# Performance work log

Hardware: AMD Instinct MI355X
Metric: run time of the kernel (lower is better)

Reference implementation:

```python
import jax, jax.numpy as jnp
import numpy as np

N_QUBITS = 8
DEPTH = 6
BATCH = 32
C = jnp.complex64

# Noise strengths from get_ibm_noise_params: constants derived from IBM Nairobi gate errors.
G1, G2 = 0.0003, 0.0065

def _amp_kraus(g):
    return [jnp.array([[1.0, 0.0], [0.0, np.sqrt(1.0 - g)]], C),
            jnp.array([[0.0, np.sqrt(g)], [0.0, 0.0]], C)]

def _phase_kraus(g):
    return [jnp.array([[1.0, 0.0], [0.0, np.sqrt(1.0 - g)]], C),
            jnp.array([[0.0, 0.0], [0.0, np.sqrt(g)]], C)]

def _depol_kraus(p):
    s0, s = np.sqrt(1.0 - p), np.sqrt(p / 3.0)
    I = np.eye(2); X = np.array([[0, 1], [1, 0]])
    Y = np.array([[0, -1j], [1j, 0]]); Z = np.diag([1, -1])
    return [jnp.array(s0 * I, C), jnp.array(s * X, C), jnp.array(s * Y, C), jnp.array(s * Z, C)]

# channels applied sequentially: amplitude damping, phase damping, depolarizing
CH_1Q = [_amp_kraus(G1 * 0.3), _phase_kraus(G1 * 0.2), _depol_kraus(G1 * 0.5)]
CH_2Q = [_amp_kraus(G2 * 0.3), _phase_kraus(G2 * 0.2), _depol_kraus(G2 * 0.5)]

CNOT4 = jnp.array([[1, 0, 0, 0], [0, 1, 0, 0], [0, 0, 0, 1], [0, 0, 1, 0]], C).reshape(2, 2, 2, 2)

# rho is a per-sample tensor of shape (2,)*(2*N): axes [0..N) are row indices, [N..2N) col indices.

def apply_1q(rho, U, w):
    # rho -> U rho U^dagger on wire w
    rho = jnp.moveaxis(jnp.tensordot(U, rho, axes=([1], [w])), 0, w)
    return jnp.moveaxis(jnp.tensordot(jnp.conj(U), rho, axes=([1], [N_QUBITS + w])), 0, N_QUBITS + w)

def apply_channel(rho, kraus, w):
    out = apply_1q(rho, kraus[0], w)
    for K in kraus[1:]:
        out = out + apply_1q(rho, K, w)
    return out

def apply_noise(rho, channels, w):
    for kraus in channels:
        rho = apply_channel(rho, kraus, w)
    return rho

def apply_cnot(rho, w):
    rho = jnp.moveaxis(jnp.tensordot(CNOT4, rho, axes=([2, 3], [w, w + 1])), [0, 1], [w, w + 1])
    return jnp.moveaxis(jnp.tensordot(jnp.conj(CNOT4), rho,
                                      axes=([2, 3], [N_QUBITS + w, N_QUBITS + w + 1])),
                        [0, 1], [N_QUBITS + w, N_QUBITS + w + 1])

def ry(t):
    c, s = jnp.cos(t / 2), jnp.sin(t / 2)
    return jnp.stack([jnp.stack([c, -s]), jnp.stack([s, c])]).astype(C)

def rz(t):
    em = jnp.exp(-0.5j * t).astype(C)  # exp(-i t/2)
    zero = jnp.zeros((), C)
    return jnp.stack([jnp.stack([em, zero]), jnp.stack([zero, jnp.conj(em)])])

def circuit(x, weights):
    # x: [N_QUBITS] angles; weights: [DEPTH, N_QUBITS, 2]
    shape = (2,) * (2 * N_QUBITS)
    rho = jnp.zeros(shape, C).at[(0,) * (2 * N_QUBITS)].set(1.0)

    def encode(rho, x):
        for i in range(N_QUBITS):
            rho = apply_1q(rho, ry(x[i]), i)
            rho = apply_noise(rho, CH_1Q, i)
        return rho

    rho = jax.checkpoint(encode)(rho, x)

    def layer(rho, wl):
        for i in range(N_QUBITS - 1):
            rho = apply_cnot(rho, i)
            rho = apply_noise(rho, CH_2Q, i)
            rho = apply_noise(rho, CH_2Q, i + 1)
        for i in range(N_QUBITS):
            rho = apply_1q(rho, ry(wl[i, 0]), i)
            rho = apply_1q(rho, rz(wl[i, 1]), i)
            rho = apply_noise(rho, CH_1Q, i)
        return rho, None

    rho, _ = jax.lax.scan(jax.checkpoint(layer), rho, weights)

    D = 2 ** N_QUBITS
    diag = jnp.diagonal(rho.reshape(D, D))
    # PauliZ on wire 0 (most significant bit in PennyLane ordering): +1 first half, -1 second half
    sign = jnp.where(jnp.arange(D) < D // 2, 1.0, -1.0)
    return jnp.real(jnp.sum(diag * sign)).astype(jnp.float32)


def setup_inputs() -> dict:
    key = jax.random.key(0)
    k1, k2 = jax.random.split(key)
    x = jax.random.normal(k1, (BATCH, N_QUBITS), dtype=jnp.float32)
    weights = jax.random.normal(k2, (DEPTH, N_QUBITS, 2), dtype=jnp.float32) * 0.1
    return {"x": x, "weights": weights}


def reference(x, weights):
    out = jax.vmap(circuit, in_axes=(0, None))(x, weights)  # [B]
    return out[:, None]  # [B, 1], matches torch .unsqueeze(1)
```

## Files before the change

### kernel.cpp

```cpp
#include <hip/hip_runtime.h>
#include <cmath>


typedef float2 cplx;
#define BATCH 32

__device__ __forceinline__ cplx cmul(cplx a, cplx b){
  return make_float2(a.x*b.x - a.y*b.y, a.x*b.y + a.y*b.x);
}
__device__ __forceinline__ cplx cadd(cplx a, cplx b){ return make_float2(a.x+b.x, a.y+b.y); }
__device__ __forceinline__ cplx lc(float a, cplx u, float b, cplx v){
  return make_float2(a*u.x + b*v.x, a*u.y + b*v.y);
}
__device__ __forceinline__ cplx sc(float a, cplx u){ return make_float2(a*u.x, a*u.y); }

struct N1C { float A,B,C,D,E; };
__device__ __forceinline__ N1C noise_coeffs(float g){
  float ga = g*0.3f, gp = g*0.2f, p = g*0.5f;
  N1C n;
  n.A = 1.0f - 2.0f*p/3.0f;
  n.D = 2.0f*p/3.0f;
  n.B = ga*n.A + n.D*(1.0f-ga);
  n.E = n.D*ga + n.A*(1.0f-ga);
  n.C = (1.0f - 4.0f*p/3.0f) * sqrtf(1.0f-ga) * sqrtf(1.0f-gp);
  return n;
}
__device__ __forceinline__ N1C mkadj(N1C n){
  N1C a; a.A=n.A; a.B=n.D; a.C=n.C; a.D=n.B; a.E=n.E; return a;
}

__device__ __forceinline__ float dpp_x1(float v){
  return __int_as_float(__builtin_amdgcn_mov_dpp(__float_as_int(v), 0xB1, 0xF, 0xF, true));
}
__device__ __forceinline__ float dpp_x3(float v){
  return __int_as_float(__builtin_amdgcn_mov_dpp(__float_as_int(v), 0x1B, 0xF, 0xF, true));
}

__device__ __forceinline__ int physof(int L){
  int rl = L >> 6;
  int rot = ((rl<<3)|(rl>>3)) & 63;
  return L ^ rot;
}
__device__ __forceinline__ constexpr int KPc(int p){
  return (p < 6) ? (1<<p) : ((1<<p) | (1 << ((p-3)%6)));
}
__device__ __forceinline__ int physB(int L){
  int rl = L >> 5;
  int rot = ((rl<<2)|(rl>>3)) & 31;
  return L ^ rot;
}
__device__ __forceinline__ constexpr int maskB(int p){
  return (p < 5) ? (1<<p) : ((1<<p) | (1 << ((p-3)%5)));
}

template<int U>
__device__ __forceinline__ int baseF(int g){
  constexpr int F[6][8] = {
    {0,0,0,0,0,0,0,0},
    {2,4,9, 3,5,8,10,11},
    {0,3,5, 4,6,9,10,11},
    {0,1,4, 5,6,7,10,11},
    {1,2,5, 0,6,7,8,11},
    {0,2,3, 1,6,7,8,9}};
  int b = 0;
  #pragma unroll
  for (int i=0;i<8;i++) b ^= (-((g>>i)&1)) & KPc(F[U][i]);
  return b;
}
template<int V>
__device__ __forceinline__ int baseBk(int g){
  constexpr int F[5][6] = {
    {0,0,0,0,0,0},
    {3,4, 2,7,8,9},
    {0,4, 3,5,8,9},
    {0,1, 4,5,6,9},
    {1,2, 0,5,6,7}};
  int b = 0;
  #pragma unroll
  for (int i=0;i<6;i++) b ^= (-((g>>i)&1)) & maskB(F[V][i]);
  return b;
}
__device__ __forceinline__ int base_s(int t){
  constexpr int P[10] = {1,2,3,9, 4,5,7,8,10,11};
  int b = 0;
  #pragma unroll
  for (int i=0;i<10;i++) b ^= (-((t>>i)&1)) & KPc(P[i]);
  return b;
}

__device__ __forceinline__ void rot_pair(cplx& v0, cplx& v1, float cy, float sy){
  cplx a=v0, b=v1;
  v0 = make_float2(cy*a.x - sy*b.x, cy*a.y - sy*b.y);
  v1 = make_float2(sy*a.x + cy*b.x, sy*a.y + cy*b.y);
}

template<int U>
__device__ __forceinline__ void fstage2(cplx* __restrict__ slab, float4 rc, int bp, int bsel,
                                        N1C n1, N1C n2, float a0, float b0, float a1, float b1){
  constexpr int KA=KPc(6+U), KB=KPc(5+U), KC=1<<U, KD=1<<(U-1);
  cplx h[8];
  #pragma unroll
  for (int i=0;i<8;i++){
    int a=(i>>2)&1, cc=(i>>1)&1, d=i&1;
    h[i] = slab[bp ^ (a?KA:0) ^ ((bsel^a)?KB:0) ^ (cc?KC:0) ^ ((d^cc)?KD:0)];
  }
  #pragma unroll
  for (int d=0;d<2;d++){
    cplx t00=h[d], t11=h[6|d];
    h[d]   = lc(n2.A,t00, n2.B,t11);
    h[6|d] = lc(n2.D,t00, n2.E,t11);
    h[2|d] = sc(n2.C, h[2|d]);
    h[4|d] = sc(n2.C, h[4|d]);
  }
  #pragma unroll
  for (int j=0;j<4;j++){
    int i0 = j<<1;
    float r0x = dpp_x1(h[i0].x),   r0y = dpp_x1(h[i0].y);
    float r1x = dpp_x1(h[i0|1].x), r1y = dpp_x1(h[i0|1].y);
    cplx h0 = h[i0], h1 = h[i0|1];
    h[i0]   = make_float2(a0*h0.x + b0*r1x, a0*h0.y + b0*r1y);
    h[i0|1] = make_float2(a1*h1.x + b1*r0x, a1*h1.y + b1*r0y);
  }
  float cy=rc.x, sy=rc.y;
  #pragma unroll
  for (int a=0;a<2;a++)
    #pragma unroll
    for (int d=0;d<2;d++) rot_pair(h[(a<<2)|d], h[(a<<2)|2|d], cy, sy);
  #pragma unroll
  for (int cc=0;cc<2;cc++)
    #pragma unroll
    for (int d=0;d<2;d++) rot_pair(h[(cc<<1)|d], h[4|(cc<<1)|d], cy, sy);
  cplx p = make_float2(rc.z, rc.w), pcj = make_float2(rc.z, -rc.w);
  #pragma unroll
  for (int d=0;d<2;d++){
    cplx t00=h[d], t11=h[6|d];
    h[d]   = lc(n1.A,t00, n1.B,t11);
    h[6|d] = lc(n1.D,t00, n1.E,t11);
    h[2|d] = cmul(p,   h[2|d]);
    h[4|d] = cmul(pcj, h[4|d]);
  }
  #pragma unroll
  for (int i=0;i<8;i++){
    int a=(i>>2)&1, cc=(i>>1)&1, d=i&1;
    slab[bp ^ (a?KA:0) ^ (bsel?KB:0) ^ (cc?KC:0) ^ (d?KD:0)] = h[i];
  }
}

__device__ __forceinline__ void redT50(cplx* __restrict__ slab, float4 rc, float g6,
                                       N1C n1, N1C n2, int t){
  constexpr int KR = KPc(6), KCb = 1;
  #pragma unroll
  for (int grp=0; grp<2; grp++){
    int bp = base_s(t | (grp<<9));
    cplx v00 = slab[bp], v01 = slab[bp^KCb], v10 = slab[bp^KR], v11 = slab[bp^KR^KCb];
    v01 = sc(g6, v01); v10 = sc(g6, v10);
    { cplx t00=v00, t11=v11;
      v00 = lc(n2.A,t00, n2.B,t11); v11 = lc(n2.D,t00, n2.E,t11);
      v01 = sc(n2.C,v01); v10 = sc(n2.C,v10); }
    float cy=rc.x, sy=rc.y;
    rot_pair(v00,v01,cy,sy); rot_pair(v10,v11,cy,sy);
    rot_pair(v00,v10,cy,sy); rot_pair(v01,v11,cy,sy);
    { cplx t00=v00, t11=v11;
      v00 = lc(n1.A,t00, n1.B,t11); v11 = lc(n1.D,t00, n1.E,t11);
      v01 = cmul(make_float2(rc.z,rc.w),  v01);
      v10 = cmul(make_float2(rc.z,-rc.w), v10); }
    slab[bp] = v00; slab[bp^KCb] = v01; slab[bp^KR] = v10; slab[bp^KR^KCb] = v11;
  }
}

template<int V>
__device__ __forceinline__ void astage_q4b(cplx* __restrict__ slab, float4 rc, int bp,
                                           int bsel, int dsel, N1C n1a, N1C n2a,
                                           float alpha, float beta){
  constexpr int KA=maskB(5+V), KB=maskB(4+V), KC=1<<V, KD=1<<(V-1);
  int fix = (bsel?KB:0) ^ (dsel?KD:0);
  cplx v[4];
  v[0] = slab[bp ^ fix];
  v[1] = slab[bp ^ fix ^ KC];
  v[2] = slab[bp ^ fix ^ KA];
  v[3] = slab[bp ^ fix ^ KA ^ KC];
  cplx p  = make_float2(rc.z, -rc.w);
  cplx pc = make_float2(rc.z,  rc.w);
  float cy=rc.x, sy=-rc.y;
  {
    cplx t00=v[0], t11=v[3];
    v[0]=lc(n1a.A,t00, n1a.B,t11);
    v[3]=lc(n1a.D,t00, n1a.E,t11);
    v[1]=cmul(p,v[1]); v[2]=cmul(pc,v[2]);
    rot_pair(v[0],v[1],cy,sy); rot_pair(v[2],v[3],cy,sy);
    rot_pair(v[0],v[2],cy,sy); rot_pair(v[1],v[3],cy,sy);
  }
  #pragma unroll
  for (int j=0;j<4;j++){
    float rx = dpp_x3(v[j].x);
    float ry = dpp_x3(v[j].y);
    v[j] = make_float2(alpha*v[j].x + beta*rx, alpha*v[j].y + beta*ry);
  }
  {
    cplx t00=v[0], t11=v[3];
    v[0]=lc(n2a.A,t00, n2a.B,t11);
    v[3]=lc(n2a.D,t00, n2a.E,t11);
    v[1]=sc(n2a.C,v[1]); v[2]=sc(n2a.C,v[2]);
  }
  int sb = bsel ? KB : 0;
  slab[bp ^ sb            ^ (dsel?KD:0)]      = v[0];
  slab[bp ^ sb ^ KC       ^ (dsel?0:KD)]      = v[1];
  slab[bp ^ (sb^KB) ^ KA  ^ (dsel?KD:0)]      = v[2];
  slab[bp ^ (sb^KB) ^ KA ^ KC ^ (dsel?0:KD)]  = v[3];
}

#define SLOT2(UU, FI, VV, BI) { \
  if (t < 512) fstage2<UU>(fslab, sS[FI], baseF<UU>(gf), bf, n1, n2, a0,b0,a1,b1); \
  else if (t < 768) astage_q4b<VV>(bslab, sS[BI], baseBk<VV>(gb), bb_, db_, n1a, n2a, alpha, beta); \
  __syncthreads(); }

__global__ __launch_bounds__(1024) void fused_kernel(const float* __restrict__ x,
                                                     const float* __restrict__ w,
                                                     float* __restrict__ out){
  __shared__ cplx fslab[4096];
  __shared__ cplx bslab[1024];
  __shared__ float4 sS[48];
  __shared__ float sm[28];
  __shared__ cplx C4s[16];
  __shared__ float red[16];
  int t = threadIdx.x, s = blockIdx.x;
  N1C n1 = noise_coeffs(0.0003f);
  N1C n2 = noise_coeffs(0.0065f);
  N1C n1a = mkadj(n1), n2a = mkadj(n2);
  int bf = t & 1, gf = t >> 1;
  float a0 = bf ? n2.C : n2.A;
  float b0 = bf ? 0.f  : n2.B;
  float a1 = bf ? n2.E : n2.C;
  float b1 = bf ? n2.D : 0.f;
  int db_ = t & 1, bb_ = (t >> 1) & 1, gb = (t >> 2) & 63;
  float alpha = (bb_==db_) ? (bb_ ? n2a.E : n2a.A) : n2a.C;
  float beta  = (bb_==db_) ? (bb_ ? n2a.D : n2a.B) : 0.f;

  if (t < 48){
    float w0=w[t*2], w1=w[t*2+1];
    sS[t] = make_float4(cosf(0.5f*w0), sinf(0.5f*w0), n1.C*cosf(w1), -n1.C*sinf(w1));
  }
  if (t < 7){
    float xv = x[s*8+t];
    float c = cosf(0.5f*xv), sn = sinf(0.5f*xv);
    float p00=c*c, p01=c*sn, p11=sn*sn;
    sm[t*4+0]=n1.A*p00+n1.B*p11; sm[t*4+1]=n1.C*p01;
    sm[t*4+2]=n1.C*p01;          sm[t*4+3]=n1.D*p00+n1.E*p11;
  }
  if (t == 63){
    float w0=w[24], w1=w[25];
    float c = cosf(0.5f*w0), sn = sinf(0.5f*w0);
    float U[2][2] = {{c,-sn},{sn,c}};
    cplx ph01 = make_float2(cosf(w1), -sinf(w1));
    cplx ph10 = make_float2(ph01.x, -ph01.y);
    cplx S4[16];
    #pragma unroll
    for (int a=0;a<2;a++)
      #pragma unroll
      for (int b=0;b<2;b++){
        int k = 2*a+b;
        float u0a=U[0][a], u0b=U[0][b], u1a=U[1][a], u1b=U[1][b];
        S4[0*4+k] = make_float2(n1.A*u0a*u0b + n1.B*u1a*u1b, 0.f);
        S4[1*4+k] = sc(n1.C*u0a*u1b, ph01);
        S4[2*4+k] = sc(n1.C*u1a*u0b, ph10);
        S4[3*4+k] = make_float2(n1.D*u0a*u0b + n1.E*u1a*u1b, 0.f);
      }
    #pragma unroll
    for (int j=0;j<4;j++){
      C4s[j*4+0] = cadd(sc(n2.A, S4[j*4+0]), sc(n2.D, S4[j*4+3]));
      C4s[j*4+1] = sc(n2.C, S4[j*4+1]);
      C4s[j*4+2] = sc(n2.C, S4[j*4+2]);
      C4s[j*4+3] = cadd(sc(n2.B, S4[j*4+0]), sc(n2.E, S4[j*4+3]));
    }
  }
  __syncthreads();
  #pragma unroll
  for (int k=0;k<4;k++){
    int L = k*1024 + t, rl = L>>6, cl = L&63;
    float v = 1.f;
    #pragma unroll
    for (int q=0;q<6;q++)
      v *= sm[q*4 + ((rl>>(5-q))&1)*2 + ((cl>>(5-q))&1)];
    fslab[physof(L)] = make_float2(v, 0.f);
  }
  if (t >= 512 && t < 768){
    int local = t - 512;
    #pragma unroll
    for (int k=0;k<4;k++){
      int o = k*256 + local, r = o>>5, c = o&31;
      bslab[physB(o)] = make_float2((r==c) ? ((r&16)? -1.f : 1.f) : 0.f, 0.f);
    }
  }
  float g6 = 2.f * sm[25];
  __syncthreads();

  SLOT2(5, 0, 4, 40)
  SLOT2(4, 1, 3, 33)
  SLOT2(3, 2, 4, 32)
  SLOT2(2, 3, 2, 26)
  SLOT2(1, 4, 3, 25)
  {
    if (t < 512) redT50(fslab, sS[5], g6, n1, n2, t);
    else if (t < 768) astage_q4b<4>(bslab, sS[24], baseBk<4>(gb), bb_, db_, n1a, n2a, alpha, beta);
    __syncthreads();
  }
  SLOT2(5, 8, 1, 19)
  SLOT2(4, 9, 2, 18)
  SLOT2(3,10, 3, 17)
  SLOT2(2,11, 4, 16)

  float acc;
  {
    int r04 = t >> 5, c04 = t & 31;
    int r03 = r04 >> 1, r4 = r04 & 1, c03 = c04 >> 1, c4 = c04 & 1;
    int rbase = c03 << 2, cbase = r03 << 2;
    #define FEL(al,be,ga,de) fslab[physof((((rbase|((al)<<1)|(be))<<6) | (cbase|((ga)<<1)|(de))))]
    cplx Q0 = cadd(FEL(0,0,0,0), FEL(0,1,0,1));
    cplx Q1 = cadd(FEL(0,0,1,1), FEL(0,1,1,0));
    cplx Q2 = cadd(FEL(1,1,0,0), FEL(1,0,0,1));
    cplx Q3 = cadd(FEL(1,1,1,1), FEL(1,0,1,0));
    #undef FEL
    int j = ((c4<<1)|r4) << 2;
    cplx z = cmul(C4s[j], Q0);
    z = cadd(z, cmul(C4s[j|1], Q1));
    z = cadd(z, cmul(C4s[j|2], Q2));
    z = cadd(z, cmul(C4s[j|3], Q3));
    cplx Ov = bslab[physB(t)];
    acc = Ov.x*z.x - Ov.y*z.y;
  }
  #pragma unroll
  for (int off=32; off>0; off>>=1) acc += __shfl_down(acc, off, 64);
  if ((t&63)==0) red[t>>6] = acc;
  __syncthreads();
  if (t==0){
    float v = 0.f;
    #pragma unroll
    for (int k=0;k<16;k++) v += red[k];
    out[s] = v;
  }
}

extern "C" void kernel_launch(void* const* d_in, const int* in_sizes, int n_in,
                              void* d_out, int out_size, void* d_ws, size_t ws_size,
                              hipStream_t stream) {
  const float* x = (const float*)d_in[0];
  const float* w = (const float*)d_in[1];
  float* out = (float*)d_out;

  fused_kernel<<<BATCH, 1024, 0, stream>>>(x, w, out);
}
```

Measured before the change: 20.11 us.

## Grow density matrices progressively qubit by qubit within single waves

Replaces the early full-size forward and backward (observable) stages with a light-cone style build-up. Each density matrix starts small, and one qubit is added at a time via tensor-product expansion, so early gates act on 4x4..32x32 matrices. That work runs inside a single wave each, using wave barriers instead of block-wide __syncthreads. Only the last few stages run on the full 64x64 slab, which removes most block-wide barriers and most redundant LDS traffic. The trade-off is that one wave does all early work serially with little parallelism, which may lengthen the critical path.

```diff
diff --git a/kernel.cpp b/kernel.cpp
--- a/kernel.cpp
+++ b/kernel.cpp
@@ -32,9 +32,6 @@
 __device__ __forceinline__ float dpp_x1(float v){
   return __int_as_float(__builtin_amdgcn_mov_dpp(__float_as_int(v), 0xB1, 0xF, 0xF, true));
 }
-__device__ __forceinline__ float dpp_x3(float v){
-  return __int_as_float(__builtin_amdgcn_mov_dpp(__float_as_int(v), 0x1B, 0xF, 0xF, true));
-}
 
 __device__ __forceinline__ int physof(int L){
   int rl = L >> 6;
@@ -43,14 +40,6 @@
 }
 __device__ __forceinline__ constexpr int KPc(int p){
   return (p < 6) ? (1<<p) : ((1<<p) | (1 << ((p-3)%6)));
-}
-__device__ __forceinline__ int physB(int L){
-  int rl = L >> 5;
-  int rot = ((rl<<2)|(rl>>3)) & 31;
-  return L ^ rot;
-}
-__device__ __forceinline__ constexpr int maskB(int p){
-  return (p < 5) ? (1<<p) : ((1<<p) | (1 << ((p-3)%5)));
 }
 
 template<int U>
@@ -67,24 +56,24 @@
   for (int i=0;i<8;i++) b ^= (-((g>>i)&1)) & KPc(F[U][i]);
   return b;
 }
-template<int V>
-__device__ __forceinline__ int baseBk(int g){
-  constexpr int F[5][6] = {
-    {0,0,0,0,0,0},
-    {3,4, 2,7,8,9},
-    {0,4, 3,5,8,9},
-    {0,1, 4,5,6,9},
-    {1,2, 0,5,6,7}};
-  int b = 0;
-  #pragma unroll
-  for (int i=0;i<6;i++) b ^= (-((g>>i)&1)) & maskB(F[V][i]);
-  return b;
-}
 __device__ __forceinline__ int base_s(int t){
   constexpr int P[10] = {1,2,3,9, 4,5,7,8,10,11};
   int b = 0;
   #pragma unroll
   for (int i=0;i<10;i++) b ^= (-((t>>i)&1)) & KPc(P[i]);
+  return b;
+}
+
+template<int B,int A0,int A1,int A2,int A3>
+__device__ __forceinline__ int dep4(int g){
+  int b = 0, gi = 0;
+  #pragma unroll
+  for (int pos=0; pos<B; ++pos){
+    if (pos!=A0 && pos!=A1 && pos!=A2 && pos!=A3){
+      b |= ((g>>gi)&1) << pos;
+      gi++;
+    }
+  }
   return b;
 }
 
@@ -92,6 +81,148 @@
   cplx a=v0, b=v1;
   v0 = make_float2(cy*a.x - sy*b.x, cy*a.y - sy*b.y);
   v1 = make_float2(sy*a.x + cy*b.x, sy*a.y + cy*b.y);
+}
+
+template<int RC,int RT,int CC,int CT>
+__device__ __forceinline__ void fwd_full(cplx* __restrict__ buf, float4 rc, int bp,
+                                         N1C n1, N1C n2){
+  constexpr int KA=1<<RC, KB=1<<RT, KC=1<<CC, KD=1<<CT;
+  cplx h[16];
+  #pragma unroll
+  for (int idx=0; idx<16; idx++){
+    int a=(idx>>3)&1, b=(idx>>2)&1, cc=(idx>>1)&1, d=idx&1;
+    h[idx] = buf[bp | (a?KA:0) | ((b^a)?KB:0) | (cc?KC:0) | ((d^cc)?KD:0)];
+  }
+  #pragma unroll
+  for (int b=0;b<2;b++)
+    #pragma unroll
+    for (int d=0;d<2;d++){
+      int i=(b<<2)|d;
+      cplx t00=h[i], t11=h[i|10];
+      h[i]    = lc(n2.A,t00, n2.B,t11);
+      h[i|10] = lc(n2.D,t00, n2.E,t11);
+      h[i|2]  = sc(n2.C, h[i|2]);
+      h[i|8]  = sc(n2.C, h[i|8]);
+    }
+  #pragma unroll
+  for (int a=0;a<2;a++)
+    #pragma unroll
+    for (int cc=0;cc<2;cc++){
+      int i=(a<<3)|(cc<<1);
+      cplx t00=h[i], t11=h[i|5];
+      h[i]   = lc(n2.A,t00, n2.B,t11);
+      h[i|5] = lc(n2.D,t00, n2.E,t11);
+      h[i|1] = sc(n2.C, h[i|1]);
+      h[i|4] = sc(n2.C, h[i|4]);
+    }
+  float cy=rc.x, sy=rc.y;
+  #pragma unroll
+  for (int a=0;a<2;a++)
+    #pragma unroll
+    for (int b=0;b<2;b++)
+      #pragma unroll
+      for (int d=0;d<2;d++){
+        int i=(a<<3)|(b<<2)|d;
+        rot_pair(h[i], h[i|2], cy, sy);
+      }
+  #pragma unroll
+  for (int b=0;b<2;b++)
+    #pragma unroll
+    for (int cc=0;cc<2;cc++)
+      #pragma unroll
+      for (int d=0;d<2;d++){
+        int i=(b<<2)|(cc<<1)|d;
+        rot_pair(h[i], h[i|8], cy, sy);
+      }
+  cplx p = make_float2(rc.z, rc.w), pcj = make_float2(rc.z, -rc.w);
+  #pragma unroll
+  for (int b=0;b<2;b++)
+    #pragma unroll
+    for (int d=0;d<2;d++){
+      int i=(b<<2)|d;
+      cplx t00=h[i], t11=h[i|10];
+      h[i]    = lc(n1.A,t00, n1.B,t11);
+      h[i|10] = lc(n1.D,t00, n1.E,t11);
+      h[i|2]  = cmul(p,   h[i|2]);
+      h[i|8]  = cmul(pcj, h[i|8]);
+    }
+  #pragma unroll
+  for (int idx=0; idx<16; idx++){
+    int a=(idx>>3)&1, b=(idx>>2)&1, cc=(idx>>1)&1, d=idx&1;
+    buf[bp | (a?KA:0) | (b?KB:0) | (cc?KC:0) | (d?KD:0)] = h[idx];
+  }
+}
+
+template<int RC,int RT,int CC,int CT>
+__device__ __forceinline__ void adj_full(cplx* __restrict__ buf, float4 rc, int bp,
+                                         N1C n1a, N1C n2a){
+  constexpr int KA=1<<RC, KB=1<<RT, KC=1<<CC, KD=1<<CT;
+  cplx h[16];
+  #pragma unroll
+  for (int idx=0; idx<16; idx++){
+    int a=(idx>>3)&1, b=(idx>>2)&1, cc=(idx>>1)&1, d=idx&1;
+    h[idx] = buf[bp | (a?KA:0) | (b?KB:0) | (cc?KC:0) | (d?KD:0)];
+  }
+  {
+    cplx p=make_float2(rc.z,-rc.w), pc=make_float2(rc.z,rc.w);
+    #pragma unroll
+    for (int b=0;b<2;b++)
+      #pragma unroll
+      for (int d=0;d<2;d++){
+        int i=(b<<2)|d;
+        cplx t00=h[i], t11=h[i|10];
+        h[i]    = lc(n1a.A,t00, n1a.B,t11);
+        h[i|10] = lc(n1a.D,t00, n1a.E,t11);
+        h[i|2]  = cmul(p,  h[i|2]);
+        h[i|8]  = cmul(pc, h[i|8]);
+      }
+    float cy=rc.x, sy=-rc.y;
+    #pragma unroll
+    for (int a=0;a<2;a++)
+      #pragma unroll
+      for (int b=0;b<2;b++)
+        #pragma unroll
+        for (int d=0;d<2;d++){
+          int i=(a<<3)|(b<<2)|d;
+          rot_pair(h[i], h[i|2], cy, sy);
+        }
+    #pragma unroll
+    for (int b=0;b<2;b++)
+      #pragma unroll
+      for (int cc=0;cc<2;cc++)
+        #pragma unroll
+        for (int d=0;d<2;d++){
+          int i=(b<<2)|(cc<<1)|d;
+          rot_pair(h[i], h[i|8], cy, sy);
+        }
+  }
+  #pragma unroll
+  for (int a=0;a<2;a++)
+    #pragma unroll
+    for (int cc=0;cc<2;cc++){
+      int i=(a<<3)|(cc<<1);
+      cplx t00=h[i], t11=h[i|5];
+      h[i]   = lc(n2a.A,t00, n2a.B,t11);
+      h[i|5] = lc(n2a.D,t00, n2a.E,t11);
+      h[i|1] = sc(n2a.C, h[i|1]);
+      h[i|4] = sc(n2a.C, h[i|4]);
+    }
+  #pragma unroll
+  for (int b=0;b<2;b++)
+    #pragma unroll
+    for (int d=0;d<2;d++){
+      int i=(b<<2)|d;
+      cplx t00=h[i], t11=h[i|10];
+      h[i]    = lc(n2a.A,t00, n2a.B,t11);
+      h[i|10] = lc(n2a.D,t00, n2a.E,t11);
+      h[i|2]  = sc(n2a.C, h[i|2]);
+      h[i|8]  = sc(n2a.C, h[i|8]);
+    }
+  #pragma unroll
+  for (int idx=0; idx<16; idx++){
+    int a=(idx>>3)&1, b=(idx>>2)&1, cc=(idx>>1)&1, d=idx&1;
+    buf[bp | (a?KA:0) | ((b^a)?KB:0) | (cc?KC:0) | ((d^cc)?KD:0)] = h[idx];
+  }
 }
 
 template<int U>
@@ -168,86 +299,123 @@
   }
 }
 
-template<int V>
-__device__ __forceinline__ void astage_q4b(cplx* __restrict__ slab, float4 rc, int bp,
-                                           int bsel, int dsel, N1C n1a, N1C n2a,
-                                           float alpha, float beta){
-  constexpr int KA=maskB(5+V), KB=maskB(4+V), KC=1<<V, KD=1<<(V-1);
-  int fix = (bsel?KB:0) ^ (dsel?KD:0);
-  cplx v[4];
-  v[0] = slab[bp ^ fix];
-  v[1] = slab[bp ^ fix ^ KC];
-  v[2] = slab[bp ^ fix ^ KA];
-  v[3] = slab[bp ^ fix ^ KA ^ KC];
-  cplx p  = make_float2(rc.z, -rc.w);
-  cplx pc = make_float2(rc.z,  rc.w);
-  float cy=rc.x, sy=-rc.y;
-  {
-    cplx t00=v[0], t11=v[3];
-    v[0]=lc(n1a.A,t00, n1a.B,t11);
-    v[3]=lc(n1a.D,t00, n1a.E,t11);
-    v[1]=cmul(p,v[1]); v[2]=cmul(pc,v[2]);
-    rot_pair(v[0],v[1],cy,sy); rot_pair(v[2],v[3],cy,sy);
-    rot_pair(v[0],v[2],cy,sy); rot_pair(v[1],v[3],cy,sy);
-  }
-  #pragma unroll
-  for (int j=0;j<4;j++){
-    float rx = dpp_x3(v[j].x);
-    float ry = dpp_x3(v[j].y);
-    v[j] = make_float2(alpha*v[j].x + beta*rx, alpha*v[j].y + beta*ry);
-  }
-  {
-    cplx t00=v[0], t11=v[3];
-    v[0]=lc(n2a.A,t00, n2a.B,t11);
-    v[3]=lc(n2a.D,t00, n2a.E,t11);
-    v[1]=sc(n2a.C,v[1]); v[2]=sc(n2a.C,v[2]);
-  }
-  int sb = bsel ? KB : 0;
-  slab[bp ^ sb            ^ (dsel?KD:0)]      = v[0];
-  slab[bp ^ sb ^ KC       ^ (dsel?0:KD)]      = v[1];
-  slab[bp ^ (sb^KB) ^ KA  ^ (dsel?KD:0)]      = v[2];
-  slab[bp ^ (sb^KB) ^ KA ^ KC ^ (dsel?0:KD)]  = v[3];
-}
-
-#define SLOT2(UU, FI, VV, BI) { \
-  if (t < 512) fstage2<UU>(fslab, sS[FI], baseF<UU>(gf), bf, n1, n2, a0,b0,a1,b1); \
-  else if (t < 768) astage_q4b<VV>(bslab, sS[BI], baseBk<VV>(gb), bb_, db_, n1a, n2a, alpha, beta); \
-  __syncthreads(); }
+#define FS(mm,qq,SSI) { \
+  constexpr int RCp = 2*(mm)-1-(qq); constexpr int CCp = (mm)-1-(qq); \
+  int NG = 1 << (2*(mm)-4); \
+  if (ln < NG) fwd_full<RCp,RCp-1,CCp,CCp-1>(fbuf, sS[SSI], \
+      dep4<2*(mm),RCp,RCp-1,CCp,CCp-1>(ln), n1, n2); \
+  __builtin_amdgcn_wave_barrier(); }
+
+#define AS(mm,qq,SBI) { \
+  constexpr int RCp = 2*(mm)-1-(qq); constexpr int CCp = (mm)-1-(qq); \
+  int NG = 1 << (2*(mm)-4); \
+  if (ln2 < NG) adj_full<RCp,RCp-1,CCp,CCp-1>(bbuf, sSb[SBI], \
+      dep4<2*(mm),RCp,RCp-1,CCp,CCp-1>(ln2), n1a, n2a); \
+  __builtin_amdgcn_wave_barrier(); }
+
+#define EXPF(mm,qn) { \
+  const int N = 1<<(2*(mm)); const int K = (N<64)?1:(N/64); \
+  cplx ov[4]; \
+  _Pragma("unroll") for (int k=0;k<K;k++){ int o=k*64+ln; ov[k] = (o<N)? fbuf[o] : make_float2(0.f,0.f); } \
+  __builtin_amdgcn_wave_barrier(); \
+  _Pragma("unroll") for (int k=0;k<K;k++){ int o=k*64+ln; if (o<N){ \
+    int r=o>>(mm), c=o&((1<<(mm))-1); \
+    _Pragma("unroll") for (int rn=0;rn<2;rn++) \
+      _Pragma("unroll") for (int cn=0;cn<2;cn++) \
+        fbuf[((r*2+rn)<<((mm)+1)) | (c*2+cn)] = sc(sm[(qn)*4+rn*2+cn], ov[k]); } } \
+  __builtin_amdgcn_wave_barrier(); }
+
+#define EXPB(mm) { \
+  const int N = 1<<(2*(mm)); const int K = (N<64)?1:(N/64); \
+  cplx ov[4]; \
+  _Pragma("unroll") for (int k=0;k<K;k++){ int o=k*64+ln2; ov[k] = (o<N)? bbuf[o] : make_float2(0.f,0.f); } \
+  __builtin_amdgcn_wave_barrier(); \
+  _Pragma("unroll") for (int k=0;k<K;k++){ int o=k*64+ln2; if (o<N){ \
+    int r=o>>(mm), c=o&((1<<(mm))-1); \
+    _Pragma("unroll") for (int rn=0;rn<2;rn++) \
+      _Pragma("unroll") for (int cn=0;cn<2;cn++) \
+        bbuf[((r*2+rn)<<((mm)+1)) | (c*2+cn)] = (rn==cn)? ov[k] : make_float2(0.f,0.f); } } \
+  __builtin_amdgcn_wave_barrier(); }
 
 __global__ __launch_bounds__(1024) void fused_kernel(const float* __restrict__ x,
                                                      const float* __restrict__ w,
                                                      float* __restrict__ out){
   __shared__ cplx fslab[4096];
-  __shared__ cplx bslab[1024];
+  __shared__ cplx fbuf[1024];
+  __shared__ cplx bbuf[1024];
   __shared__ float4 sS[48];
+  __shared__ float4 sSb[10];
   __shared__ float sm[28];
   __shared__ cplx C4s[16];
   __shared__ float red[16];
   int t = threadIdx.x, s = blockIdx.x;
+  int wave = t >> 6;
   N1C n1 = noise_coeffs(0.0003f);
   N1C n2 = noise_coeffs(0.0065f);
-  N1C n1a = mkadj(n1), n2a = mkadj(n2);
   int bf = t & 1, gf = t >> 1;
   float a0 = bf ? n2.C : n2.A;
   float b0 = bf ? 0.f  : n2.B;
   float a1 = bf ? n2.E : n2.C;
   float b1 = bf ? n2.D : 0.f;
-  int db_ = t & 1, bb_ = (t >> 1) & 1, gb = (t >> 2) & 63;
-  float alpha = (bb_==db_) ? (bb_ ? n2a.E : n2a.A) : n2a.C;
-  float beta  = (bb_==db_) ? (bb_ ? n2a.D : n2a.B) : 0.f;
-
-  if (t < 48){
-    float w0=w[t*2], w1=w[t*2+1];
-    sS[t] = make_float4(cosf(0.5f*w0), sinf(0.5f*w0), n1.C*cosf(w1), -n1.C*sinf(w1));
-  }
-  if (t < 7){
-    float xv = x[s*8+t];
-    float c = cosf(0.5f*xv), sn = sinf(0.5f*xv);
-    float p00=c*c, p01=c*sn, p11=sn*sn;
-    sm[t*4+0]=n1.A*p00+n1.B*p11; sm[t*4+1]=n1.C*p01;
-    sm[t*4+2]=n1.C*p01;          sm[t*4+3]=n1.D*p00+n1.E*p11;
-  }
-  if (t == 63){
+
+  if (wave == 0){
+    int ln = t;
+    if (ln < 48){
+      float w0=w[ln*2], w1=w[ln*2+1];
+      sS[ln] = make_float4(cosf(0.5f*w0), sinf(0.5f*w0), n1.C*cosf(w1), -n1.C*sinf(w1));
+    }
+    if (ln < 7){
+      float xv = x[s*8+ln];
+      float c = cosf(0.5f*xv), sn = sinf(0.5f*xv);
+      float p00=c*c, p01=c*sn, p11=sn*sn;
+      sm[ln*4+0]=n1.A*p00+n1.B*p11; sm[ln*4+1]=n1.C*p01;
+      sm[ln*4+2]=n1.C*p01;          sm[ln*4+3]=n1.D*p00+n1.E*p11;
+    }
+    __builtin_amdgcn_wave_barrier();
+    if (ln < 16){
+      int r = ln>>2, c = ln&3;
+      fbuf[ln] = make_float2(sm[((r>>1)&1)*2+((c>>1)&1)] * sm[4+(r&1)*2+(c&1)], 0.f);
+    }
+    __builtin_amdgcn_wave_barrier();
+    FS(2,0,0)
+    EXPF(2,2)
+    FS(3,1,1)
+    FS(3,0,8)
+    EXPF(3,3)
+    FS(4,2,2)
+    FS(4,1,9)
+    EXPF(4,4)
+    FS(5,3,3)
+    FS(5,2,10)
+  } else if (wave == 1){
+    int ln2 = t - 64;
+    N1C n1a = mkadj(n1), n2a = mkadj(n2);
+    if (ln2 < 10){
+      constexpr int LQ[10][2] = {{5,0},{4,1},{4,0},{3,2},{3,1},{3,0},{2,3},{2,2},{2,1},{2,0}};
+      int l = LQ[ln2][0], q = LQ[ln2][1];
+      float w0=w[(l*8+q)*2], w1=w[(l*8+q)*2+1];
+      sSb[ln2] = make_float4(cosf(0.5f*w0), sinf(0.5f*w0), n1.C*cosf(w1), -n1.C*sinf(w1));
+    }
+    __builtin_amdgcn_wave_barrier();
+    if (ln2 < 16){
+      int r = ln2>>2, c = ln2&3;
+      bbuf[ln2] = make_float2((r==c) ? ((r&2)? -1.f : 1.f) : 0.f, 0.f);
+    }
+    __builtin_amdgcn_wave_barrier();
+    AS(2,0,0)
+    EXPB(2)
+    AS(3,1,1)
+    AS(3,0,2)
+    EXPB(3)
+    AS(4,2,3)
+    AS(4,1,4)
+    AS(4,0,5)
+    EXPB(4)
+    AS(5,3,6)
+    AS(5,2,7)
+    AS(5,1,8)
+    AS(5,0,9)
+  } else if (t == 128){
     float w0=w[24], w1=w[25];
     float c = cosf(0.5f*w0), sn = sinf(0.5f*w0);
     float U[2][2] = {{c,-sn},{sn,c}};
@@ -274,40 +442,21 @@
     }
   }
   __syncthreads();
+
+  float g6 = 2.f * sm[25];
   #pragma unroll
   for (int k=0;k<4;k++){
     int L = k*1024 + t, rl = L>>6, cl = L&63;
-    float v = 1.f;
-    #pragma unroll
-    for (int q=0;q<6;q++)
-      v *= sm[q*4 + ((rl>>(5-q))&1)*2 + ((cl>>(5-q))&1)];
-    fslab[physof(L)] = make_float2(v, 0.f);
-  }
-  if (t >= 512 && t < 768){
-    int local = t - 512;
-    #pragma unroll
-    for (int k=0;k<4;k++){
-      int o = k*256 + local, r = o>>5, c = o&31;
-      bslab[physB(o)] = make_float2((r==c) ? ((r&16)? -1.f : 1.f) : 0.f, 0.f);
-    }
-  }
-  float g6 = 2.f * sm[25];
+    cplx fv = fbuf[(rl>>1)*32 + (cl>>1)];
+    fslab[physof(L)] = sc(sm[20 + (rl&1)*2 + (cl&1)], fv);
+  }
   __syncthreads();
-
-  SLOT2(5, 0, 4, 40)
-  SLOT2(4, 1, 3, 33)
-  SLOT2(3, 2, 4, 32)
-  SLOT2(2, 3, 2, 26)
-  SLOT2(1, 4, 3, 25)
-  {
-    if (t < 512) redT50(fslab, sS[5], g6, n1, n2, t);
-    else if (t < 768) astage_q4b<4>(bslab, sS[24], baseBk<4>(gb), bb_, db_, n1a, n2a, alpha, beta);
-    __syncthreads();
-  }
-  SLOT2(5, 8, 1, 19)
-  SLOT2(4, 9, 2, 18)
-  SLOT2(3,10, 3, 17)
-  SLOT2(2,11, 4, 16)
+  if (t < 512) fstage2<1>(fslab, sS[4], baseF<1>(gf), bf, n1, n2, a0,b0,a1,b1);
+  __syncthreads();
+  if (t < 512) redT50(fslab, sS[5], g6, n1, n2, t);
+  __syncthreads();
+  if (t < 512) fstage2<2>(fslab, sS[11], baseF<2>(gf), bf, n1, n2, a0,b0,a1,b1);
+  __syncthreads();
 
   float acc;
   {
@@ -325,7 +474,7 @@
     z = cadd(z, cmul(C4s[j|1], Q1));
     z = cadd(z, cmul(C4s[j|2], Q2));
     z = cadd(z, cmul(C4s[j|3], Q3));
-    cplx Ov = bslab[physB(t)];
+    cplx Ov = bbuf[t];
     acc = Ov.x*z.x - Ov.y*z.y;
   }
   #pragma unroll
```

After: 20.93 us. 4.0% more time.
